# Performance work log

Measured on AMD Instinct MI355X. Metric: run time of the kernel, lower is better.

Reference implementation:

```python
import jax, jax.numpy as jnp
import numpy as np

HEAD_SIZE = 64


def setup_inputs() -> dict:
    key = jax.random.key(0)
    k1, k2, k3, k4 = jax.random.split(key, 4)
    x = jax.random.normal(k1, (4, 4096, 1024), dtype=jnp.float32)
    Wk = jax.random.normal(k2, (1024, HEAD_SIZE), dtype=jnp.float32) * 0.02
    Wq = jax.random.normal(k3, (1024, HEAD_SIZE), dtype=jnp.float32) * 0.02
    Wv = jax.random.normal(k4, (1024, HEAD_SIZE), dtype=jnp.float32) * 0.02
    return {"x": x, "Wk": Wk, "Wq": Wq, "Wv": Wv}


def reference(x, Wk, Wq, Wv):
    # x: [B, S, D]; projections (Linear without bias): x @ W -> [B, S, H]
    k = jnp.einsum('bsd,dh->bsh', x, Wk)
    q = jnp.einsum('bsd,dh->bsh', x, Wq)
    v = jnp.einsum('bsd,dh->bsh', x, Wv)
    scale = 1.0 / np.sqrt(HEAD_SIZE).astype(np.float32)
    z = jnp.einsum('bqh,bkh->bqk', q, k) * scale  # [B, S, S]
    S = x.shape[1]
    causal = jnp.tril(jnp.ones((S, S), dtype=bool))
    z = jnp.where(causal, z, -jnp.inf)
    z = jax.nn.softmax(z, axis=2)
    return jnp.einsum('bqk,bkh->bqh', z, v)
```

## Files before the change

kernel.cpp:

```cpp
#include <hip/hip_runtime.h>
#include <hip/hip_bf16.h>
#include <stdint.h>
#include <math.h>

typedef __attribute__((ext_vector_type(8))) short short8;
typedef __attribute__((ext_vector_type(4))) short short4v;
typedef __attribute__((ext_vector_type(4))) float float4v;

#define MFMA16(a,b,c) __builtin_amdgcn_mfma_f32_16x16x32_bf16((a),(b),(c),0,0,0)

__device__ __forceinline__ short bf16r(float f) {
  union { float f; uint32_t u; } v; v.f = f;
  uint32_t r = v.u + 0x7fffu + ((v.u >> 16) & 1u);
  return (short)(r >> 16);
}
__device__ __forceinline__ float bf2f(short s) {
  union { float f; uint32_t u; } v; v.u = ((uint32_t)(uint16_t)s) << 16;
  return v.f;
}
__device__ __forceinline__ uint32_t cvtpk(float a, float b) {
  uint32_t r;
  asm("v_cvt_pk_bf16_f32 %0, %1, %2" : "=v"(r) : "v"(a), "v"(b));
  return r;
}

__device__ __forceinline__ void gld_lds16(void* lds, const void* g) {
  __builtin_amdgcn_global_load_lds(
      (const __attribute__((address_space(1))) uint32_t*)g,
      (__attribute__((address_space(3))) uint32_t*)lds, 16, 0, 0);
}

__global__ __launch_bounds__(256) void prep_wt(
    const float* __restrict__ Wk, const float* __restrict__ Wq,
    const float* __restrict__ Wv, short* __restrict__ WT) {
  __shared__ float tile[64][65];
  const int w = blockIdx.y;
  const int k0 = blockIdx.x * 64;
  const float* W = (w == 0) ? Wk : (w == 1) ? Wq : Wv;
  const int tid = threadIdx.x;
#pragma unroll
  for (int i = 0; i < 16; ++i) {
    int e = i * 256 + tid;
    int kk = e >> 6, hh = e & 63;
    tile[kk][hh] = W[(size_t)(k0 + kk) * 64 + hh];
  }
  __syncthreads();
#pragma unroll
  for (int i = 0; i < 16; ++i) {
    int e = i * 256 + tid;
    int hh = e >> 6, kk = e & 63;
    WT[(size_t)w * 65536 + hh * 1024 + k0 + kk] = bf16r(tile[kk][hh]);
  }
}

__global__ __launch_bounds__(512, 4) void proj_kernel(
    const float* __restrict__ x, const short* __restrict__ WT,
    short* __restrict__ Kg, short* __restrict__ Qg, short* __restrict__ Vt) {
  __shared__ __align__(16) short xs[2][32][72];
  __shared__ __align__(16) short wts[2][192 * 64];
  const int tid = threadIdx.x;
  const int lane = tid & 63;
  const int w = tid >> 6;
  const int c = lane & 15;
  const int sl = lane >> 4;
  const int mh = w & 1;
  const int nh = w >> 1;
  const int m0 = blockIdx.x * 32;

  float4v acc[3];
#pragma unroll
  for (int ni = 0; ni < 3; ++ni) acc[ni] = (float4v){0.f, 0.f, 0.f, 0.f};

  const int srow = tid >> 4;
  const int scol = (tid & 15) * 4;
  const float* xrow = x + (size_t)(m0 + srow) * 1024 + scol;

#define PSTAGE_WT(buf, kk)                                                    \
  _Pragma("unroll") for (int rr = 0; rr < 3; ++rr) {                          \
    const int chunk = rr * 512 + tid;                                         \
    const int n = chunk >> 3;                                                 \
    const int cc = chunk & 7;                                                 \
    gld_lds16(wts[buf] + chunk * 8,                                           \
              WT + (size_t)n * 1024 + (kk) + ((cc ^ (n & 7)) * 8));           \
  }
#define PWRITE_X(buf)                                                         \
  {                                                                           \
    short4v hx;                                                               \
    hx.x = bf16r(xr.x); hx.y = bf16r(xr.y);                                   \
    hx.z = bf16r(xr.z); hx.w = bf16r(xr.w);                                   \
    *(short4v*)(&xs[buf][srow][scol]) = hx;                                   \
  }

  float4v xr = *(const float4v*)(xrow);
  float4v xn = *(const float4v*)(xrow + 64);

  PSTAGE_WT(0, 0)
  PWRITE_X(0)
  __syncthreads();

  int cur = 0;
  for (int it = 0; it < 16; ++it) {
    const int k0 = it * 64;
    if (it + 1 < 16) {
      PSTAGE_WT(cur ^ 1, k0 + 64)
      xr = xn;
      PWRITE_X(cur ^ 1)
      if (it + 2 < 16) xn = *(const float4v*)(xrow + k0 + 128);
    }
    short8 a0 = *(const short8*)(&xs[cur][mh * 16 + c][sl * 8]);
    short8 a1 = *(const short8*)(&xs[cur][mh * 16 + c][32 + sl * 8]);
#pragma unroll
    for (int ni = 0; ni < 3; ++ni) {
      const int rw = (nh * 3 + ni) * 16 + c;
      short8 b0 = *(const short8*)(wts[cur] + rw * 64 + ((sl ^ (rw & 7)) * 8));
      short8 b1 = *(const short8*)(wts[cur] + rw * 64 + (((sl + 4) ^ (rw & 7)) * 8));
      acc[ni] = MFMA16(a0, b0, acc[ni]);
      acc[ni] = MFMA16(a1, b1, acc[ni]);
    }
    __syncthreads();
    cur ^= 1;
  }
#undef PSTAGE_WT
#undef PWRITE_X

  const int b = m0 >> 12;
  const int s_base = m0 & 4095;
  const float QSCALE = 0.18033688011112042f;
#pragma unroll
  for (int ni = 0; ni < 3; ++ni) {
    const int nt = nh * 3 + ni;
    const int wsel = nt >> 2;
    const int h = (nt & 3) * 16 + c;
    const int q_local = mh * 16 + sl * 4;
    if (wsel == 2) {
      short4v pv;
      pv.x = bf16r(acc[ni].x); pv.y = bf16r(acc[ni].y);
      pv.z = bf16r(acc[ni].z); pv.w = bf16r(acc[ni].w);
      *(short4v*)(Vt + (size_t)(b * 64 + h) * 4096 + s_base + q_local) = pv;
    } else if (wsel == 1) {
#pragma unroll
      for (int i = 0; i < 4; ++i)
        Qg[(size_t)(m0 + q_local + i) * 64 + h] = bf16r(acc[ni][i] * QSCALE);
    } else {
#pragma unroll
      for (int i = 0; i < 4; ++i)
        Kg[(size_t)(m0 + q_local + i) * 64 + h] = bf16r(acc[ni][i]);
    }
  }
}

#define SLOT_BYTES 16896
__global__ __launch_bounds__(256, 4)
__attribute__((amdgpu_waves_per_eu(4, 4)))
void attn_kernel(
    const short* __restrict__ Qg, const short* __restrict__ Kg,
    const short* __restrict__ Vt, float* __restrict__ out,
    char* __restrict__ part, int split) {
  __shared__ __align__(16) short Ks[2][64 * 64];
  __shared__ __align__(16) short Vs[2][64 * 64];
  const int tid = threadIdx.x;
  const int lane = tid & 63;
  const int w = tid >> 6;
  const int c = lane & 15;
  const int sl = lane >> 4;

  int g, ch, b, uu = 0;
  if (split) {
    const int lin = (blockIdx.x & 7) * 136 + (blockIdx.x >> 3);
    b = lin / 272;
    uu = lin - b * 272;
    g = (int)(2.0f * sqrtf((float)uu));
    while (((g + 2) >> 1) * ((g + 3) >> 1) <= uu) ++g;
    while (((g + 1) >> 1) * ((g + 2) >> 1) > uu) --g;
    ch = uu - ((g + 1) >> 1) * ((g + 2) >> 1);
  } else { g = blockIdx.x; b = blockIdx.y; ch = 0; }
  const int T = 2 * (g + 1);
  const int c0 = ch * 4;
  const int c1 = (!split || c0 + 4 > T) ? T : c0 + 4;
  const int nch = split ? ((g >> 1) + 1) : 1;
  const int qw = g * 128 + w * 32;

  const short* Kb = Kg + (size_t)b * 4096 * 64;
  const short* Vb = Vt + (size_t)b * 64 * 4096;

  short8 aq[2][2];
#pragma unroll
  for (int qf = 0; qf < 2; ++qf) {
    const short* qp = Qg + (size_t)(b * 4096 + qw + qf * 16 + c) * 64 + sl * 8;
    aq[qf][0] = *(const short8*)(qp);
    aq[qf][1] = *(const short8*)(qp + 32);
  }

  float4v o[2][4];
#pragma unroll
  for (int qf = 0; qf < 2; ++qf)
#pragma unroll
    for (int ht = 0; ht < 4; ++ht) o[qf][ht] = (float4v){0.f, 0.f, 0.f, 0.f};
  float lsum[2] = {0.f, 0.f};

#define STAGE(buf, t)                                                        \
  {                                                                          \
    const int kv0s = (t) * 64;                                               \
    _Pragma("unroll")                                                        \
    for (int j = 0; j < 2; ++j) {                                            \
      const int chunk = j * 256 + tid;                                       \
      const int rw = chunk >> 3;                                             \
      const int scol = ((chunk & 7) ^ (rw & 7)) * 8;                         \
      gld_lds16(Ks[buf] + chunk * 8, Kb + (size_t)(kv0s + rw) * 64 + scol);  \
      gld_lds16(Vs[buf] + chunk * 8, Vb + (size_t)rw * 4096 + kv0s + scol);  \
    }                                                                        \
  }

  STAGE(0, c0)
  __syncthreads();

  const int srcA = c + 32 * (sl & 1);
  const int srcB = srcA + 16;

  int cur = 0;
  for (int t = c0; t < c1; ++t) {
    const int kv0 = t * 64;
    if (t + 1 < c1) STAGE(cur ^ 1, t + 1)

    const short* KsC = Ks[cur];
    const short* VsC = Vs[cur];
    const bool maskTile = (kv0 + 63 > qw);

    uint32_t tpk[2][4][2];
    __builtin_amdgcn_s_setprio(1);
#pragma unroll
    for (int nt = 0; nt < 4; ++nt) {
      const int rw = nt * 16 + c;
      short8 kb0 = *(const short8*)(KsC + rw * 64 + ((sl ^ (rw & 7)) * 8));
      short8 kb1 = *(const short8*)(KsC + rw * 64 + (((sl + 4) ^ (rw & 7)) * 8));
#pragma unroll
      for (int qf = 0; qf < 2; ++qf) {
        float4v z = {0.f, 0.f, 0.f, 0.f};
        z = MFMA16(kb0, aq[qf][0], z);
        z = MFMA16(kb1, aq[qf][1], z);
        if (maskTile) {
          const int qg = qw + qf * 16 + c;
#pragma unroll
          for (int i = 0; i < 4; ++i) {
            const int kvg = kv0 + nt * 16 + sl * 4 + i;
            z[i] = (kvg <= qg) ? z[i] : -1e30f;
          }
        }
        const float p0 = exp2f(z[0]);
        const float p1 = exp2f(z[1]);
        const float p2 = exp2f(z[2]);
        const float p3 = exp2f(z[3]);
        lsum[qf] += (p0 + p1) + (p2 + p3);
        tpk[qf][nt][0] = cvtpk(p0, p1);
        tpk[qf][nt][1] = cvtpk(p2, p3);
      }
    }
    __builtin_amdgcn_s_setprio(0);

    short8 ap[2][2];
#pragma unroll
    for (int qf = 0; qf < 2; ++qf)
#pragma unroll
      for (int f = 0; f < 2; ++f) {
        const uint32_t q0a = __shfl((int)tpk[qf][2 * f][0], srcA);
        const uint32_t q0b = __shfl((int)tpk[qf][2 * f + 1][0], srcA);
        const uint32_t q1a = __shfl((int)tpk[qf][2 * f][1], srcA);
        const uint32_t q1b = __shfl((int)tpk[qf][2 * f + 1][1], srcA);
        const uint32_t q2a = __shfl((int)tpk[qf][2 * f][0], srcB);
        const uint32_t q2b = __shfl((int)tpk[qf][2 * f + 1][0], srcB);
        const uint32_t q3a = __shfl((int)tpk[qf][2 * f][1], srcB);
        const uint32_t q3b = __shfl((int)tpk[qf][2 * f + 1][1], srcB);
        const bool lo = (sl < 2);
        union { uint32_t u[4]; short8 s8; } ua;
        ua.u[0] = lo ? q0a : q0b;
        ua.u[1] = lo ? q1a : q1b;
        ua.u[2] = lo ? q2a : q2b;
        ua.u[3] = lo ? q3a : q3b;
        ap[qf][f] = ua.s8;
      }

    __builtin_amdgcn_s_setprio(1);
#pragma unroll
    for (int ht = 0; ht < 4; ++ht) {
      const int rw = ht * 16 + c;
      short8 vb0 = *(const short8*)(VsC + rw * 64 + ((sl ^ (rw & 7)) * 8));
      short8 vb1 = *(const short8*)(VsC + rw * 64 + (((sl + 4) ^ (rw & 7)) * 8));
#pragma unroll
      for (int qf = 0; qf < 2; ++qf) {
        o[qf][ht] = MFMA16(ap[qf][0], vb0, o[qf][ht]);
        o[qf][ht] = MFMA16(ap[qf][1], vb1, o[qf][ht]);
      }
    }
    __builtin_amdgcn_s_setprio(0);

    if (t + 1 < c1) __syncthreads();
    cur ^= 1;
  }
#undef STAGE

  float rsum[2];
#pragma unroll
  for (int qf = 0; qf < 2; ++qf) {
    float r = lsum[qf];
    r += __shfl_xor(r, 16);
    r += __shfl_xor(r, 32);
    rsum[qf] = r;
  }

  if (nch == 1) {
    float inv[2][4];
#pragma unroll
    for (int qf = 0; qf < 2; ++qf)
#pragma unroll
      for (int i = 0; i < 4; ++i)
        inv[qf][i] = 1.0f / __shfl(rsum[qf], sl * 4 + i);
#pragma unroll
    for (int qf = 0; qf < 2; ++qf)
#pragma unroll
      for (int ht = 0; ht < 4; ++ht)
#pragma unroll
        for (int i = 0; i < 4; ++i) {
          const int q = qw + qf * 16 + sl * 4 + i;
          out[(size_t)(b * 4096 + q) * 64 + ht * 16 + c] = o[qf][ht][i] * inv[qf][i];
        }
  } else {
    short* sp = (short*)(part + (size_t)(b * 272 + uu) * SLOT_BYTES);
    float* lp = (float*)(sp + 8192);
#pragma unroll
    for (int qf = 0; qf < 2; ++qf)
#pragma unroll
      for (int ht = 0; ht < 4; ++ht)
#pragma unroll
        for (int i = 0; i < 4; ++i) {
          const int row = w * 32 + qf * 16 + sl * 4 + i;
          sp[row * 64 + ht * 16 + c] = bf16r(o[qf][ht][i]);
        }
    if (sl == 0) {
#pragma unroll
      for (int qf = 0; qf < 2; ++qf)
        lp[w * 32 + qf * 16 + c] = rsum[qf];
    }
  }
}

__global__ __launch_bounds__(256) void combine_kernel(
    const char* __restrict__ part, float* __restrict__ out) {
  const int g = blockIdx.x;
  const int b = blockIdx.y;
  const int N = (g >> 1) + 1;
  if (N == 1) return;
  const int F = ((g + 1) >> 1) * ((g + 2) >> 1);
  const char* base = part + (size_t)(b * 272 + F) * SLOT_BYTES;
  const int r = blockIdx.z * 32 + (threadIdx.x >> 3);
  const int cb = (threadIdx.x & 7) * 8;

  float L = 0.f;
  float acc[8];
#pragma unroll
  for (int k = 0; k < 8; ++k) acc[k] = 0.f;
  for (int i = 0; i < N; ++i) {
    const short* sp = (const short*)(base + (size_t)i * SLOT_BYTES);
    L += ((const float*)(sp + 8192))[r];
    short8 v = *(const short8*)(sp + r * 64 + cb);
#pragma unroll
    for (int j = 0; j < 8; ++j) acc[j] += bf2f(v[j]);
  }
  const float inv = 1.0f / L;
  float* op = out + (size_t)(b * 4096 + g * 128 + r) * 64 + cb;
  float4v r0 = {acc[0] * inv, acc[1] * inv, acc[2] * inv, acc[3] * inv};
  float4v r1 = {acc[4] * inv, acc[5] * inv, acc[6] * inv, acc[7] * inv};
  *(float4v*)(op) = r0;
  *(float4v*)(op + 4) = r1;
}

extern "C" void kernel_launch(void* const* d_in, const int* in_sizes, int n_in,
                              void* d_out, int out_size, void* d_ws, size_t ws_size,
                              hipStream_t stream) {
  const float* x  = (const float*)d_in[0];
  const float* Wk = (const float*)d_in[1];
  const float* Wq = (const float*)d_in[2];
  const float* Wv = (const float*)d_in[3];

  char* ws = (char*)d_ws;
  short* WT = (short*)ws;
  short* Kg = (short*)(ws + 393216);
  short* Qg = (short*)(ws + 393216 + 2097152);
  short* Vt = (short*)(ws + 393216 + 2 * 2097152);
  const size_t part_off = 393216 + 3 * 2097152;
  char* part = ws + part_off;

  const int split = (ws_size >= part_off + (size_t)1088 * SLOT_BYTES) ? 1 : 0;

  prep_wt<<<dim3(16, 3), dim3(256), 0, stream>>>(Wk, Wq, Wv, WT);
  proj_kernel<<<dim3(512), dim3(512), 0, stream>>>(x, WT, Kg, Qg, Vt);
  attn_kernel<<<split ? dim3(1088) : dim3(32, 4), dim3(256), 0, stream>>>(
      Qg, Kg, Vt, (float*)d_out, part, split);
  if (split)
    combine_kernel<<<dim3(32, 4, 4), dim3(256), 0, stream>>>(part, (float*)d_out);
}
```

Measured before the change: 70.52 us.

## Use 8 waves of 16 query rows each in attention blocks

```diff
diff --git a/kernel.cpp b/kernel.cpp
--- a/kernel.cpp
+++ b/kernel.cpp
@@ -150,9 +150,7 @@
 }
 
 #define SLOT_BYTES 16896
-__global__ __launch_bounds__(256, 4)
-__attribute__((amdgpu_waves_per_eu(4, 4)))
-void attn_kernel(
+__global__ __launch_bounds__(512, 8) void attn_kernel(
     const short* __restrict__ Qg, const short* __restrict__ Kg,
     const short* __restrict__ Vt, float* __restrict__ out,
     char* __restrict__ part, int split) {
@@ -178,37 +176,30 @@
   const int c0 = ch * 4;
   const int c1 = (!split || c0 + 4 > T) ? T : c0 + 4;
   const int nch = split ? ((g >> 1) + 1) : 1;
-  const int qw = g * 128 + w * 32;
+  const int qw = g * 128 + w * 16;
 
   const short* Kb = Kg + (size_t)b * 4096 * 64;
   const short* Vb = Vt + (size_t)b * 64 * 4096;
 
-  short8 aq[2][2];
-#pragma unroll
-  for (int qf = 0; qf < 2; ++qf) {
-    const short* qp = Qg + (size_t)(b * 4096 + qw + qf * 16 + c) * 64 + sl * 8;
-    aq[qf][0] = *(const short8*)(qp);
-    aq[qf][1] = *(const short8*)(qp + 32);
-  }
-
-  float4v o[2][4];
-#pragma unroll
-  for (int qf = 0; qf < 2; ++qf)
-#pragma unroll
-    for (int ht = 0; ht < 4; ++ht) o[qf][ht] = (float4v){0.f, 0.f, 0.f, 0.f};
-  float lsum[2] = {0.f, 0.f};
+  short8 aq0, aq1;
+  {
+    const short* qp = Qg + (size_t)(b * 4096 + qw + c) * 64 + sl * 8;
+    aq0 = *(const short8*)(qp);
+    aq1 = *(const short8*)(qp + 32);
+  }
+
+  float4v o[4];
+#pragma unroll
+  for (int ht = 0; ht < 4; ++ht) o[ht] = (float4v){0.f, 0.f, 0.f, 0.f};
+  float lsum = 0.f;
 
 #define STAGE(buf, t)                                                        \
   {                                                                          \
     const int kv0s = (t) * 64;                                               \
-    _Pragma("unroll")                                                        \
-    for (int j = 0; j < 2; ++j) {                                            \
-      const int chunk = j * 256 + tid;                                       \
-      const int rw = chunk >> 3;                                             \
-      const int scol = ((chunk & 7) ^ (rw & 7)) * 8;                         \
-      gld_lds16(Ks[buf] + chunk * 8, Kb + (size_t)(kv0s + rw) * 64 + scol);  \
-      gld_lds16(Vs[buf] + chunk * 8, Vb + (size_t)rw * 4096 + kv0s + scol);  \
-    }                                                                        \
+    const int rw = tid >> 3;                                                 \
+    const int scol = ((tid & 7) ^ (rw & 7)) * 8;                             \
+    gld_lds16(Ks[buf] + tid * 8, Kb + (size_t)(kv0s + rw) * 64 + scol);      \
+    gld_lds16(Vs[buf] + tid * 8, Vb + (size_t)rw * 4096 + kv0s + scol);      \
   }
 
   STAGE(0, c0)
@@ -224,60 +215,63 @@
 
     const short* KsC = Ks[cur];
     const short* VsC = Vs[cur];
-    const bool maskTile = (kv0 + 63 > qw);
-
-    uint32_t tpk[2][4][2];
+
+    float4v s[4];
     __builtin_amdgcn_s_setprio(1);
 #pragma unroll
     for (int nt = 0; nt < 4; ++nt) {
       const int rw = nt * 16 + c;
       short8 kb0 = *(const short8*)(KsC + rw * 64 + ((sl ^ (rw & 7)) * 8));
       short8 kb1 = *(const short8*)(KsC + rw * 64 + (((sl + 4) ^ (rw & 7)) * 8));
-#pragma unroll
-      for (int qf = 0; qf < 2; ++qf) {
-        float4v z = {0.f, 0.f, 0.f, 0.f};
-        z = MFMA16(kb0, aq[qf][0], z);
-        z = MFMA16(kb1, aq[qf][1], z);
-        if (maskTile) {
-          const int qg = qw + qf * 16 + c;
-#pragma unroll
-          for (int i = 0; i < 4; ++i) {
-            const int kvg = kv0 + nt * 16 + sl * 4 + i;
-            z[i] = (kvg <= qg) ? z[i] : -1e30f;
-          }
+      float4v z = {0.f, 0.f, 0.f, 0.f};
+      z = MFMA16(kb0, aq0, z);
+      z = MFMA16(kb1, aq1, z);
+      s[nt] = z;
+    }
+    __builtin_amdgcn_s_setprio(0);
+
+    if (kv0 + 63 > qw) {
+      const int qg = qw + c;
+#pragma unroll
+      for (int nt = 0; nt < 4; ++nt)
+#pragma unroll
+        for (int i = 0; i < 4; ++i) {
+          const int kvg = kv0 + nt * 16 + sl * 4 + i;
+          s[nt][i] = (kvg <= qg) ? s[nt][i] : -1e30f;
         }
-        const float p0 = exp2f(z[0]);
-        const float p1 = exp2f(z[1]);
-        const float p2 = exp2f(z[2]);
-        const float p3 = exp2f(z[3]);
-        lsum[qf] += (p0 + p1) + (p2 + p3);
-        tpk[qf][nt][0] = cvtpk(p0, p1);
-        tpk[qf][nt][1] = cvtpk(p2, p3);
-      }
-    }
-    __builtin_amdgcn_s_setprio(0);
-
-    short8 ap[2][2];
-#pragma unroll
-    for (int qf = 0; qf < 2; ++qf)
-#pragma unroll
-      for (int f = 0; f < 2; ++f) {
-        const uint32_t q0a = __shfl((int)tpk[qf][2 * f][0], srcA);
-        const uint32_t q0b = __shfl((int)tpk[qf][2 * f + 1][0], srcA);
-        const uint32_t q1a = __shfl((int)tpk[qf][2 * f][1], srcA);
-        const uint32_t q1b = __shfl((int)tpk[qf][2 * f + 1][1], srcA);
-        const uint32_t q2a = __shfl((int)tpk[qf][2 * f][0], srcB);
-        const uint32_t q2b = __shfl((int)tpk[qf][2 * f + 1][0], srcB);
-        const uint32_t q3a = __shfl((int)tpk[qf][2 * f][1], srcB);
-        const uint32_t q3b = __shfl((int)tpk[qf][2 * f + 1][1], srcB);
-        const bool lo = (sl < 2);
-        union { uint32_t u[4]; short8 s8; } ua;
-        ua.u[0] = lo ? q0a : q0b;
-        ua.u[1] = lo ? q1a : q1b;
-        ua.u[2] = lo ? q2a : q2b;
-        ua.u[3] = lo ? q3a : q3b;
-        ap[qf][f] = ua.s8;
-      }
+    }
+
+    uint32_t tpk[4][2];
+#pragma unroll
+    for (int nt = 0; nt < 4; ++nt) {
+      const float p0 = exp2f(s[nt][0]);
+      const float p1 = exp2f(s[nt][1]);
+      const float p2 = exp2f(s[nt][2]);
+      const float p3 = exp2f(s[nt][3]);
+      lsum += (p0 + p1) + (p2 + p3);
+      tpk[nt][0] = cvtpk(p0, p1);
+      tpk[nt][1] = cvtpk(p2, p3);
+    }
+
+    short8 ap[2];
+#pragma unroll
+    for (int f = 0; f < 2; ++f) {
+      const uint32_t q0a = __shfl((int)tpk[2 * f][0], srcA);
+      const uint32_t q0b = __shfl((int)tpk[2 * f + 1][0], srcA);
+      const uint32_t q1a = __shfl((int)tpk[2 * f][1], srcA);
+      const uint32_t q1b = __shfl((int)tpk[2 * f + 1][1], srcA);
+      const uint32_t q2a = __shfl((int)tpk[2 * f][0], srcB);
+      const uint32_t q2b = __shfl((int)tpk[2 * f + 1][0], srcB);
+      const uint32_t q3a = __shfl((int)tpk[2 * f][1], srcB);
+      const uint32_t q3b = __shfl((int)tpk[2 * f + 1][1], srcB);
+      const bool lo = (sl < 2);
+      union { uint32_t u[4]; short8 s8; } ua;
+      ua.u[0] = lo ? q0a : q0b;
+      ua.u[1] = lo ? q1a : q1b;
+      ua.u[2] = lo ? q2a : q2b;
+      ua.u[3] = lo ? q3a : q3b;
+      ap[f] = ua.s8;
+    }
 
     __builtin_amdgcn_s_setprio(1);
 #pragma unroll
@@ -285,11 +279,8 @@
       const int rw = ht * 16 + c;
       short8 vb0 = *(const short8*)(VsC + rw * 64 + ((sl ^ (rw & 7)) * 8));
       short8 vb1 = *(const short8*)(VsC + rw * 64 + (((sl + 4) ^ (rw & 7)) * 8));
-#pragma unroll
-      for (int qf = 0; qf < 2; ++qf) {
-        o[qf][ht] = MFMA16(ap[qf][0], vb0, o[qf][ht]);
-        o[qf][ht] = MFMA16(ap[qf][1], vb1, o[qf][ht]);
-      }
+      o[ht] = MFMA16(ap[0], vb0, o[ht]);
+      o[ht] = MFMA16(ap[1], vb1, o[ht]);
     }
     __builtin_amdgcn_s_setprio(0);
 
@@ -298,48 +289,33 @@
   }
 #undef STAGE
 
-  float rsum[2];
-#pragma unroll
-  for (int qf = 0; qf < 2; ++qf) {
-    float r = lsum[qf];
-    r += __shfl_xor(r, 16);
-    r += __shfl_xor(r, 32);
-    rsum[qf] = r;
-  }
+  float rsum = lsum;
+  rsum += __shfl_xor(rsum, 16);
+  rsum += __shfl_xor(rsum, 32);
 
   if (nch == 1) {
-    float inv[2][4];
-#pragma unroll
-    for (int qf = 0; qf < 2; ++qf)
-#pragma unroll
-      for (int i = 0; i < 4; ++i)
-        inv[qf][i] = 1.0f / __shfl(rsum[qf], sl * 4 + i);
-#pragma unroll
-    for (int qf = 0; qf < 2; ++qf)
-#pragma unroll
-      for (int ht = 0; ht < 4; ++ht)
-#pragma unroll
-        for (int i = 0; i < 4; ++i) {
-          const int q = qw + qf * 16 + sl * 4 + i;
-          out[(size_t)(b * 4096 + q) * 64 + ht * 16 + c] = o[qf][ht][i] * inv[qf][i];
-        }
+    float inv[4];
+#pragma unroll
+    for (int i = 0; i < 4; ++i)
+      inv[i] = 1.0f / __shfl(rsum, sl * 4 + i);
+#pragma unroll
+    for (int ht = 0; ht < 4; ++ht)
+#pragma unroll
+      for (int i = 0; i < 4; ++i) {
+        const int q = qw + sl * 4 + i;
+        out[(size_t)(b * 4096 + q) * 64 + ht * 16 + c] = o[ht][i] * inv[i];
+      }
   } else {
     short* sp = (short*)(part + (size_t)(b * 272 + uu) * SLOT_BYTES);
     float* lp = (float*)(sp + 8192);
 #pragma unroll
-    for (int qf = 0; qf < 2; ++qf)
-#pragma unroll
-      for (int ht = 0; ht < 4; ++ht)
-#pragma unroll
-        for (int i = 0; i < 4; ++i) {
-          const int row = w * 32 + qf * 16 + sl * 4 + i;
-          sp[row * 64 + ht * 16 + c] = bf16r(o[qf][ht][i]);
-        }
-    if (sl == 0) {
-#pragma unroll
-      for (int qf = 0; qf < 2; ++qf)
-        lp[w * 32 + qf * 16 + c] = rsum[qf];
-    }
+    for (int ht = 0; ht < 4; ++ht)
+#pragma unroll
+      for (int i = 0; i < 4; ++i) {
+        const int row = w * 16 + sl * 4 + i;
+        sp[row * 64 + ht * 16 + c] = bf16r(o[ht][i]);
+      }
+    if (sl == 0) lp[w * 16 + c] = rsum;
   }
 }
 
@@ -393,7 +369,7 @@
 
   prep_wt<<<dim3(16, 3), dim3(256), 0, stream>>>(Wk, Wq, Wv, WT);
   proj_kernel<<<dim3(512), dim3(512), 0, stream>>>(x, WT, Kg, Qg, Vt);
-  attn_kernel<<<split ? dim3(1088) : dim3(32, 4), dim3(256), 0, stream>>>(
+  attn_kernel<<<split ? dim3(1088) : dim3(32, 4), dim3(512), 0, stream>>>(
       Qg, Kg, Vt, (float*)d_out, part, split);
   if (split)
     combine_kernel<<<dim3(32, 4, 4), dim3(256), 0, stream>>>(part, (float*)d_out);
```

Result: slower. 75.75 us (+7.4%).
